# Optimization experiments

Measured on AMD Instinct MI355X. Metric: run time of the kernel, lower is better.

Reference implementation:

```python
import jax, jax.numpy as jnp
import numpy as np

N_NODES = 100000


def setup_inputs() -> dict:
    key = jax.random.key(0)
    k1, k2, k3, k4 = jax.random.split(key, 4)
    h = jax.random.normal(k1, (N_NODES, 128), dtype=jnp.float32)
    src = jax.random.randint(k2, (1600000,), 0, N_NODES, dtype=jnp.int32)
    dst = jax.random.randint(k3, (1600000,), 0, N_NODES, dtype=jnp.int32)
    # Linear params (PyTorch default init scale ~ 1/sqrt(in_feats))
    W = jax.random.normal(k4, (128, 128), dtype=jnp.float32) * (1.0 / np.sqrt(128.0))
    b = jnp.zeros((128,), dtype=jnp.float32)
    return {"h": h, "src": src, "dst": dst, "W": W, "b": b}


def reference(h, src, dst, W, b):
    # fn.copy_src: gather source-node features per edge  [E, F]
    msgs = h[src]
    # fn.sum: scatter-add messages into destination nodes  [N, F]
    agg = jax.ops.segment_sum(msgs, dst, num_segments=h.shape[0])
    # NodeUpdateModule: linear + relu
    out = agg @ W.T + b
    return jax.nn.relu(out)
```

## Files before the change

### kernel.cpp

```cpp
#include <hip/hip_runtime.h>

#define F     128
#define NPB   128
#define NPBS  7
#define CAP   6144
#define NBMAX 1024
#define SPLIT 4
#define NPG   32
#define ECAP  1024
#define BR    64
#define KC    32

typedef short bf16x8 __attribute__((ext_vector_type(8)));
typedef float f32x4  __attribute__((ext_vector_type(4)));

__device__ __forceinline__ unsigned short f32_to_bf16_rne(float x) {
    unsigned u = __float_as_uint(x);
    u += 0x7fffu + ((u >> 16) & 1u);
    return (unsigned short)(u >> 16);
}
__device__ __forceinline__ float bf16_to_f32(unsigned short u) {
    return __uint_as_float((unsigned)u << 16);
}

__global__ __launch_bounds__(256) void conv_w_kernel(
        const float* __restrict__ Wf, unsigned short* __restrict__ Wb, int n4) {
    int i = blockIdx.x * blockDim.x + threadIdx.x;
    if (i < n4) {
        float4 v = *(const float4*)(Wf + 4 * (long)i);
        ushort4 o;
        o.x = f32_to_bf16_rne(v.x);
        o.y = f32_to_bf16_rne(v.y);
        o.z = f32_to_bf16_rne(v.z);
        o.w = f32_to_bf16_rne(v.w);
        *(ushort4*)(Wb + 4 * (long)i) = o;
    }
}

__global__ __launch_bounds__(256) void gemm_h_kernel(
        const float* __restrict__ h,
        const unsigned short* __restrict__ Wb,
        unsigned short* __restrict__ hp,
        int n_rows) {
    const int wave = (blockIdx.x * 256 + threadIdx.x) >> 6;
    const int lane = threadIdx.x & 63;
    const int m0 = wave * 16;
    if (m0 >= n_rows) return;
    const int mn   = lane & 15;
    const int quad = lane >> 4;

    const int rowc = min(m0 + mn, n_rows - 1);
    const float* arow = h + (long)rowc * F + quad * 8;

    bf16x8 afr[4];
    #pragma unroll
    for (int kk = 0; kk < 4; ++kk) {
        float4 p0 = *(const float4*)(arow + kk * 32);
        float4 p1 = *(const float4*)(arow + kk * 32 + 4);
        bf16x8 f;
        f[0] = (short)f32_to_bf16_rne(p0.x);
        f[1] = (short)f32_to_bf16_rne(p0.y);
        f[2] = (short)f32_to_bf16_rne(p0.z);
        f[3] = (short)f32_to_bf16_rne(p0.w);
        f[4] = (short)f32_to_bf16_rne(p1.x);
        f[5] = (short)f32_to_bf16_rne(p1.y);
        f[6] = (short)f32_to_bf16_rne(p1.z);
        f[7] = (short)f32_to_bf16_rne(p1.w);
        afr[kk] = f;
    }

    f32x4 acc[8];
    #pragma unroll
    for (int t = 0; t < 8; ++t) acc[t] = (f32x4){0.f, 0.f, 0.f, 0.f};

    #pragma unroll
    for (int kk = 0; kk < 4; ++kk) {
        #pragma unroll
        for (int t = 0; t < 8; ++t) {
            const unsigned short* wp = Wb + (long)(t * 16 + mn) * F + kk * 32 + quad * 8;
            bf16x8 bfr = *(const bf16x8*)wp;
            acc[t] = __builtin_amdgcn_mfma_f32_16x16x32_bf16(afr[kk], bfr, acc[t], 0, 0, 0);
        }
    }

    #pragma unroll
    for (int t = 0; t < 8; ++t) {
        const int col = t * 16 + mn;
        #pragma unroll
        for (int r = 0; r < 4; ++r) {
            const int orow = m0 + quad * 4 + r;
            if (orow < n_rows)
                hp[(long)orow * F + col] = f32_to_bf16_rne(acc[t][r]);
        }
    }
}

__global__ __launch_bounds__(256) void build_buckets_kernel(
        const int* __restrict__ src,
        const int* __restrict__ dst,
        const unsigned short* __restrict__ hp,
        int* __restrict__ bcnt,
        int* __restrict__ bpool,
        float* __restrict__ out,
        int n_edges, int NB) {
    __shared__ int hist[NBMAX];
    __shared__ int basep[NBMAX];

    const int per = (n_edges + gridDim.x - 1) / gridDim.x;
    const int lo = blockIdx.x * per;
    const int hi = min(n_edges, lo + per);
    const int tid = threadIdx.x;

    for (int i = tid; i < NB; i += 256) hist[i] = 0;
    __syncthreads();

    for (int i = lo + tid; i < hi; i += 256)
        atomicAdd(&hist[dst[i] >> NPBS], 1);
    __syncthreads();

    for (int i = tid; i < NB; i += 256) {
        int c = hist[i];
        basep[i] = c ? atomicAdd(&bcnt[i], c) : 0;
        hist[i] = 0;
    }
    __syncthreads();

    for (int i = lo + tid; i < hi; i += 256) {
        int d = dst[i], s = src[i];
        int bk = d >> NPBS;
        int p = atomicAdd(&hist[bk], 1);
        long idx = (long)basep[bk] + p;
        if (idx < CAP) {
            bpool[(long)bk * CAP + idx] = ((d & (NPB - 1)) << 20) | s;
        } else {
            float* o = out + (long)d * F;
            const unsigned short* hr = hp + (long)s * F;
            for (int k = 0; k < F; ++k) unsafeAtomicAdd(o + k, bf16_to_f32(hr[k]));
        }
    }
}

__global__ __launch_bounds__(256) void bucket_gather_kernel(
        const unsigned short* __restrict__ hp,
        const int* __restrict__ bcnt,
        const int* __restrict__ bpool,
        const float* __restrict__ bias,
        float* __restrict__ out,
        int n_nodes) {
    __shared__ int ecnt[NPG];
    __shared__ int eofs[NPG];
    __shared__ int epos[NPG];
    __shared__ int elist[ECAP];
    __shared__ int sflag;

    const int bkt = blockIdx.x >> 2;
    const int qr  = blockIdx.x & 3;
    const int q0  = qr * NPG;
    const int nb0 = (bkt << NPBS) + q0;
    const int tid = threadIdx.x;

    const int total = bcnt[bkt];
    const int count = min(total, CAP);
    const int* bp = bpool + (long)bkt * CAP;

    if (tid < NPG) ecnt[tid] = 0;
    if (tid == 0) sflag = 0;
    __syncthreads();

    for (int i = tid; i < count; i += 256) {
        int nl = (bp[i] >> 20) - q0;
        if ((unsigned)nl < NPG) atomicAdd(&ecnt[nl], 1);
    }
    __syncthreads();

    if (tid < NPG) {
        int a = ecnt[tid];
        int s = a;
        #pragma unroll
        for (int d = 1; d < NPG; d <<= 1) {
            int t = __shfl_up(s, d);
            if (tid >= d) s += t;
        }
        eofs[tid] = s - a;
        epos[tid] = s - a;
    }
    __syncthreads();

    for (int i = tid; i < count; i += 256) {
        int e = bp[i];
        int nl = (e >> 20) - q0;
        if ((unsigned)nl < NPG) {
            int p = atomicAdd(&epos[nl], 1);
            int s = e & 0xFFFFF;
            if (p < ECAP) {
                elist[p] = s;
            } else {
                sflag = 1;
                float* o = out + ((long)((bkt << NPBS) + (e >> 20))) * F;
                const unsigned short* hr = hp + (long)s * F;
                for (int k = tid & 0; k < F; ++k)
                    unsafeAtomicAdd(o + k, bf16_to_f32(hr[k]));
            }
        }
    }
    __syncthreads();

    const int lane = tid & 63;
    const int w = tid >> 6;
    const bool ovf = (total > CAP) || (sflag != 0);
    const float2 bv = *(const float2*)(bias + (lane << 1));

    for (int nl = w; nl < NPG; nl += 4) {
        int n = nb0 + nl;
        if (n >= n_nodes) break;
        const int beg = eofs[nl];
        const int dend = min(beg + ecnt[nl], ECAP);

        float ax = 0.f, ay = 0.f;
        for (int i = beg; i < dend; i += 8) {
            unsigned v[8]; bool val[8];
            #pragma unroll
            for (int j = 0; j < 8; ++j) {
                val[j] = (i + j) < dend;
                int sid = elist[val[j] ? i + j : beg];
                v[j] = *(const unsigned*)(hp + ((long)sid << NPBS) + (lane << 1));
            }
            #pragma unroll
            for (int j = 0; j < 8; ++j) {
                if (val[j]) {
                    ax += __uint_as_float(v[j] << 16);
                    ay += __uint_as_float(v[j] & 0xffff0000u);
                }
            }
        }

        float* o = out + ((long)n << NPBS) + (lane << 1);
        if (ovf) {
            ax += unsafeAtomicAdd(o, 0.f);
            ay += unsafeAtomicAdd(o + 1, 0.f);
        }
        float rx = fmaxf(ax + bv.x, 0.f);
        float ry = fmaxf(ay + bv.y, 0.f);
        *(float2*)o = make_float2(rx, ry);
    }
}

__global__ void scatter_add_kernel(const float* __restrict__ h,
                                   const int* __restrict__ src,
                                   const int* __restrict__ dst,
                                   float* __restrict__ agg,
                                   long total) {
    long stride = (long)gridDim.x * blockDim.x;
    for (long i = (long)blockIdx.x * blockDim.x + threadIdx.x; i < total; i += stride) {
        int e    = (int)(i >> 5);
        int lane = (int)(i & 31);
        int s = src[e];
        int d = dst[e];
        float4 v = *(const float4*)(h + (long)s * F + (lane << 2));
        float* o = agg + (long)d * F + (lane << 2);
        unsafeAtomicAdd(o + 0, v.x);
        unsafeAtomicAdd(o + 1, v.y);
        unsafeAtomicAdd(o + 2, v.z);
        unsafeAtomicAdd(o + 3, v.w);
    }
}

__global__ __launch_bounds__(256) void gemm_bias_relu_inplace(
        float* __restrict__ out,
        const float* __restrict__ W,
        const float* __restrict__ bias,
        int n_rows) {
    __shared__ __align__(16) float a_t[KC][BR + 4];
    __shared__ __align__(16) float w_t[KC][F + 4];
    const int tid = threadIdx.x;
    const int tx = tid & 15;
    const int ty = tid >> 4;
    const int row0 = blockIdx.x * BR;
    float acc[4][8];
    #pragma unroll
    for (int i = 0; i < 4; ++i)
        #pragma unroll
        for (int j = 0; j < 8; ++j) acc[i][j] = 0.f;
    for (int kc = 0; kc < F; kc += KC) {
        #pragma unroll
        for (int p = 0; p < 2; ++p) {
            int q = tid + p * 256, r = q >> 3, kq = q & 7;
            int row = row0 + r;
            float4 v = make_float4(0.f, 0.f, 0.f, 0.f);
            if (row < n_rows) v = *(const float4*)(out + (long)row * F + kc + (kq << 2));
            a_t[kq * 4 + 0][r] = v.x; a_t[kq * 4 + 1][r] = v.y;
            a_t[kq * 4 + 2][r] = v.z; a_t[kq * 4 + 3][r] = v.w;
        }
        #pragma unroll
        for (int p = 0; p < 4; ++p) {
            int q = tid + p * 256, j = q >> 3, kq = q & 7;
            float4 v = *(const float4*)(W + (long)j * F + kc + (kq << 2));
            w_t[kq * 4 + 0][j] = v.x; w_t[kq * 4 + 1][j] = v.y;
            w_t[kq * 4 + 2][j] = v.z; w_t[kq * 4 + 3][j] = v.w;
        }
        __syncthreads();
        #pragma unroll
        for (int k = 0; k < KC; ++k) {
            float4 av = *(const float4*)&a_t[k][ty << 2];
            float4 w0 = *(const float4*)&w_t[k][tx << 2];
            float4 w1 = *(const float4*)&w_t[k][64 + (tx << 2)];
            float a4[4] = {av.x, av.y, av.z, av.w};
            float wv[8] = {w0.x, w0.y, w0.z, w0.w, w1.x, w1.y, w1.z, w1.w};
            #pragma unroll
            for (int i = 0; i < 4; ++i)
                #pragma unroll
                for (int j = 0; j < 8; ++j) acc[i][j] += a4[i] * wv[j];
        }
        __syncthreads();
    }
    float4 b0 = *(const float4*)(bias + (tx << 2));
    float4 b1 = *(const float4*)(bias + 64 + (tx << 2));
    #pragma unroll
    for (int i = 0; i < 4; ++i) {
        int row = row0 + (ty << 2) + i;
        if (row < n_rows) {
            float4 r0, r1;
            r0.x = fmaxf(acc[i][0] + b0.x, 0.f); r0.y = fmaxf(acc[i][1] + b0.y, 0.f);
            r0.z = fmaxf(acc[i][2] + b0.z, 0.f); r0.w = fmaxf(acc[i][3] + b0.w, 0.f);
            r1.x = fmaxf(acc[i][4] + b1.x, 0.f); r1.y = fmaxf(acc[i][5] + b1.y, 0.f);
            r1.z = fmaxf(acc[i][6] + b1.z, 0.f); r1.w = fmaxf(acc[i][7] + b1.w, 0.f);
            *(float4*)(out + (long)row * F + (tx << 2)) = r0;
            *(float4*)(out + (long)row * F + 64 + (tx << 2)) = r1;
        }
    }
}

extern "C" void kernel_launch(void* const* d_in, const int* in_sizes, int n_in,
                              void* d_out, int out_size, void* d_ws, size_t ws_size,
                              hipStream_t stream) {
    const float* h   = (const float*)d_in[0];
    const int*   src = (const int*)d_in[1];
    const int*   dst = (const int*)d_in[2];
    const float* W   = (const float*)d_in[3];
    const float* b   = (const float*)d_in[4];
    float* out = (float*)d_out;

    const int n_nodes = in_sizes[0] / F;
    const int n_edges = in_sizes[1];
    const int NB = (n_nodes + NPB - 1) >> NPBS;

    const size_t off_bcnt  = 0;
    const size_t off_bpool = 4096;
    const size_t off_hp    = off_bpool + (size_t)NB * CAP * sizeof(int);
    const size_t off_wb    = off_hp + (size_t)n_nodes * F * sizeof(unsigned short);
    const size_t need      = off_wb + (size_t)F * F * sizeof(unsigned short);

    if (ws_size >= need && n_nodes < (1 << 20) && NB <= NBMAX) {
        int* bcnt  = (int*)((char*)d_ws + off_bcnt);
        int* bpool = (int*)((char*)d_ws + off_bpool);
        unsigned short* hp = (unsigned short*)((char*)d_ws + off_hp);
        unsigned short* Wb = (unsigned short*)((char*)d_ws + off_wb);

        hipMemsetAsync(bcnt, 0, (size_t)NB * sizeof(int), stream);
        hipMemsetAsync(out, 0, (size_t)out_size * sizeof(float), stream);

        conv_w_kernel<<<(F * F / 4 + 255) / 256, 256, 0, stream>>>(W, Wb, F * F / 4);

        const int ggrid = (n_nodes + 63) / 64;
        gemm_h_kernel<<<ggrid, 256, 0, stream>>>(h, Wb, hp, n_nodes);

        build_buckets_kernel<<<512, 256, 0, stream>>>(
            src, dst, hp, bcnt, bpool, out, n_edges, NB);

        bucket_gather_kernel<<<NB * SPLIT, 256, 0, stream>>>(
            hp, bcnt, bpool, b, out, n_nodes);
    } else {
        hipMemsetAsync(out, 0, (size_t)out_size * sizeof(float), stream);
        scatter_add_kernel<<<16384, 256, 0, stream>>>(
            h, src, dst, out, (long)n_edges * 32);
        const int gblocks = (n_nodes + BR - 1) / BR;
        gemm_bias_relu_inplace<<<gblocks, 256, 0, stream>>>(out, W, b, n_nodes);
    }
}
```

Baseline: 263.8 us.

## Fuse bucket build with bf16 GEMM and defer overflow edges to gather

```diff
diff --git a/kernel.cpp b/kernel.cpp
--- a/kernel.cpp
+++ b/kernel.cpp
@@ -5,9 +5,11 @@
 #define NPBS  7
 #define CAP   6144
 #define NBMAX 1024
-#define SPLIT 4
-#define NPG   32
+#define NBUILD 512
+#define SPLIT 8
+#define NPG   16
 #define ECAP  1024
+#define OCAP  131072
 #define BR    64
 #define KC    32
 
@@ -19,123 +21,114 @@
     u += 0x7fffu + ((u >> 16) & 1u);
     return (unsigned short)(u >> 16);
 }
-__device__ __forceinline__ float bf16_to_f32(unsigned short u) {
-    return __uint_as_float((unsigned)u << 16);
-}
-
-__global__ __launch_bounds__(256) void conv_w_kernel(
-        const float* __restrict__ Wf, unsigned short* __restrict__ Wb, int n4) {
-    int i = blockIdx.x * blockDim.x + threadIdx.x;
-    if (i < n4) {
-        float4 v = *(const float4*)(Wf + 4 * (long)i);
-        ushort4 o;
-        o.x = f32_to_bf16_rne(v.x);
-        o.y = f32_to_bf16_rne(v.y);
-        o.z = f32_to_bf16_rne(v.z);
-        o.w = f32_to_bf16_rne(v.w);
-        *(ushort4*)(Wb + 4 * (long)i) = o;
-    }
-}
-
-__global__ __launch_bounds__(256) void gemm_h_kernel(
+
+__global__ __launch_bounds__(256) void fused_build_gemm(
         const float* __restrict__ h,
-        const unsigned short* __restrict__ Wb,
-        unsigned short* __restrict__ hp,
-        int n_rows) {
-    const int wave = (blockIdx.x * 256 + threadIdx.x) >> 6;
-    const int lane = threadIdx.x & 63;
-    const int m0 = wave * 16;
-    if (m0 >= n_rows) return;
-    const int mn   = lane & 15;
-    const int quad = lane >> 4;
-
-    const int rowc = min(m0 + mn, n_rows - 1);
-    const float* arow = h + (long)rowc * F + quad * 8;
-
-    bf16x8 afr[4];
-    #pragma unroll
-    for (int kk = 0; kk < 4; ++kk) {
-        float4 p0 = *(const float4*)(arow + kk * 32);
-        float4 p1 = *(const float4*)(arow + kk * 32 + 4);
-        bf16x8 f;
-        f[0] = (short)f32_to_bf16_rne(p0.x);
-        f[1] = (short)f32_to_bf16_rne(p0.y);
-        f[2] = (short)f32_to_bf16_rne(p0.z);
-        f[3] = (short)f32_to_bf16_rne(p0.w);
-        f[4] = (short)f32_to_bf16_rne(p1.x);
-        f[5] = (short)f32_to_bf16_rne(p1.y);
-        f[6] = (short)f32_to_bf16_rne(p1.z);
-        f[7] = (short)f32_to_bf16_rne(p1.w);
-        afr[kk] = f;
-    }
-
-    f32x4 acc[8];
-    #pragma unroll
-    for (int t = 0; t < 8; ++t) acc[t] = (f32x4){0.f, 0.f, 0.f, 0.f};
-
-    #pragma unroll
-    for (int kk = 0; kk < 4; ++kk) {
-        #pragma unroll
-        for (int t = 0; t < 8; ++t) {
-            const unsigned short* wp = Wb + (long)(t * 16 + mn) * F + kk * 32 + quad * 8;
-            bf16x8 bfr = *(const bf16x8*)wp;
-            acc[t] = __builtin_amdgcn_mfma_f32_16x16x32_bf16(afr[kk], bfr, acc[t], 0, 0, 0);
-        }
-    }
-
-    #pragma unroll
-    for (int t = 0; t < 8; ++t) {
-        const int col = t * 16 + mn;
-        #pragma unroll
-        for (int r = 0; r < 4; ++r) {
-            const int orow = m0 + quad * 4 + r;
-            if (orow < n_rows)
-                hp[(long)orow * F + col] = f32_to_bf16_rne(acc[t][r]);
-        }
-    }
-}
-
-__global__ __launch_bounds__(256) void build_buckets_kernel(
+        const float* __restrict__ W,
         const int* __restrict__ src,
         const int* __restrict__ dst,
-        const unsigned short* __restrict__ hp,
         int* __restrict__ bcnt,
         int* __restrict__ bpool,
-        float* __restrict__ out,
-        int n_edges, int NB) {
+        uint2* __restrict__ ovf_list,
+        unsigned short* __restrict__ hp,
+        int n_edges, int n_nodes, int NB) {
     __shared__ int hist[NBMAX];
     __shared__ int basep[NBMAX];
 
-    const int per = (n_edges + gridDim.x - 1) / gridDim.x;
-    const int lo = blockIdx.x * per;
-    const int hi = min(n_edges, lo + per);
-    const int tid = threadIdx.x;
-
-    for (int i = tid; i < NB; i += 256) hist[i] = 0;
-    __syncthreads();
-
-    for (int i = lo + tid; i < hi; i += 256)
-        atomicAdd(&hist[dst[i] >> NPBS], 1);
-    __syncthreads();
-
-    for (int i = tid; i < NB; i += 256) {
-        int c = hist[i];
-        basep[i] = c ? atomicAdd(&bcnt[i], c) : 0;
-        hist[i] = 0;
-    }
-    __syncthreads();
-
-    for (int i = lo + tid; i < hi; i += 256) {
-        int d = dst[i], s = src[i];
-        int bk = d >> NPBS;
-        int p = atomicAdd(&hist[bk], 1);
-        long idx = (long)basep[bk] + p;
-        if (idx < CAP) {
-            bpool[(long)bk * CAP + idx] = ((d & (NPB - 1)) << 20) | s;
-        } else {
-            float* o = out + (long)d * F;
-            const unsigned short* hr = hp + (long)s * F;
-            for (int k = 0; k < F; ++k) unsafeAtomicAdd(o + k, bf16_to_f32(hr[k]));
+    if (blockIdx.x < NBUILD) {
+        const int per = (n_edges + NBUILD - 1) / NBUILD;
+        const int lo = blockIdx.x * per;
+        const int hi = min(n_edges, lo + per);
+        const int tid = threadIdx.x;
+
+        for (int i = tid; i < NB; i += 256) hist[i] = 0;
+        __syncthreads();
+
+        for (int i = lo + tid; i < hi; i += 256)
+            atomicAdd(&hist[dst[i] >> NPBS], 1);
+        __syncthreads();
+
+        for (int i = tid; i < NB; i += 256) {
+            int c = hist[i];
+            basep[i] = c ? atomicAdd(&bcnt[i], c) : 0;
+            hist[i] = 0;
+        }
+        __syncthreads();
+
+        int* ovf_cnt = bcnt + NBMAX;
+        for (int i = lo + tid; i < hi; i += 256) {
+            int d = dst[i], s = src[i];
+            int bk = d >> NPBS;
+            int p = atomicAdd(&hist[bk], 1);
+            long idx = (long)basep[bk] + p;
+            if (idx < CAP) {
+                bpool[(long)bk * CAP + idx] = ((d & (NPB - 1)) << 20) | s;
+            } else {
+                int op = atomicAdd(ovf_cnt, 1);
+                if (op < OCAP) ovf_list[op] = make_uint2((unsigned)s, (unsigned)d);
+            }
+        }
+    } else {
+        const int wave = ((blockIdx.x - NBUILD) * 256 + (int)threadIdx.x) >> 6;
+        const int lane = threadIdx.x & 63;
+        const int m0 = wave * 16;
+        if (m0 >= n_nodes) return;
+        const int mn   = lane & 15;
+        const int quad = lane >> 4;
+
+        const int rowc = min(m0 + mn, n_nodes - 1);
+        const float* arow = h + (long)rowc * F + quad * 8;
+
+        bf16x8 afr[4];
+        #pragma unroll
+        for (int kk = 0; kk < 4; ++kk) {
+            float4 p0 = *(const float4*)(arow + kk * 32);
+            float4 p1 = *(const float4*)(arow + kk * 32 + 4);
+            bf16x8 f;
+            f[0] = (short)f32_to_bf16_rne(p0.x);
+            f[1] = (short)f32_to_bf16_rne(p0.y);
+            f[2] = (short)f32_to_bf16_rne(p0.z);
+            f[3] = (short)f32_to_bf16_rne(p0.w);
+            f[4] = (short)f32_to_bf16_rne(p1.x);
+            f[5] = (short)f32_to_bf16_rne(p1.y);
+            f[6] = (short)f32_to_bf16_rne(p1.z);
+            f[7] = (short)f32_to_bf16_rne(p1.w);
+            afr[kk] = f;
+        }
+
+        f32x4 acc[8];
+        #pragma unroll
+        for (int t = 0; t < 8; ++t) acc[t] = (f32x4){0.f, 0.f, 0.f, 0.f};
+
+        #pragma unroll
+        for (int kk = 0; kk < 4; ++kk) {
+            #pragma unroll
+            for (int t = 0; t < 8; ++t) {
+                const float* wp = W + (long)(t * 16 + mn) * F + kk * 32 + quad * 8;
+                float4 q0 = *(const float4*)wp;
+                float4 q1 = *(const float4*)(wp + 4);
+                bf16x8 bfr;
+                bfr[0] = (short)f32_to_bf16_rne(q0.x);
+                bfr[1] = (short)f32_to_bf16_rne(q0.y);
+                bfr[2] = (short)f32_to_bf16_rne(q0.z);
+                bfr[3] = (short)f32_to_bf16_rne(q0.w);
+                bfr[4] = (short)f32_to_bf16_rne(q1.x);
+                bfr[5] = (short)f32_to_bf16_rne(q1.y);
+                bfr[6] = (short)f32_to_bf16_rne(q1.z);
+                bfr[7] = (short)f32_to_bf16_rne(q1.w);
+                acc[t] = __builtin_amdgcn_mfma_f32_16x16x32_bf16(afr[kk], bfr, acc[t], 0, 0, 0);
+            }
+        }
+
+        #pragma unroll
+        for (int t = 0; t < 8; ++t) {
+            const int col = t * 16 + mn;
+            #pragma unroll
+            for (int r = 0; r < 4; ++r) {
+                const int orow = m0 + quad * 4 + r;
+                if (orow < n_nodes)
+                    hp[(long)orow * F + col] = f32_to_bf16_rne(acc[t][r]);
+            }
         }
     }
 }
@@ -143,6 +136,7 @@
 __global__ __launch_bounds__(256) void bucket_gather_kernel(
         const unsigned short* __restrict__ hp,
         const int* __restrict__ bcnt,
+        const uint2* __restrict__ ovf_list,
         const int* __restrict__ bpool,
         const float* __restrict__ bias,
         float* __restrict__ out,
@@ -151,11 +145,9 @@
     __shared__ int eofs[NPG];
     __shared__ int epos[NPG];
     __shared__ int elist[ECAP];
-    __shared__ int sflag;
-
-    const int bkt = blockIdx.x >> 2;
-    const int qr  = blockIdx.x & 3;
-    const int q0  = qr * NPG;
+
+    const int bkt = blockIdx.x >> 3;
+    const int q0  = (blockIdx.x & 7) * NPG;
     const int nb0 = (bkt << NPBS) + q0;
     const int tid = threadIdx.x;
 
@@ -164,7 +156,6 @@
     const int* bp = bpool + (long)bkt * CAP;
 
     if (tid < NPG) ecnt[tid] = 0;
-    if (tid == 0) sflag = 0;
     __syncthreads();
 
     for (int i = tid; i < count; i += 256) {
@@ -174,8 +165,7 @@
     __syncthreads();
 
     if (tid < NPG) {
-        int a = ecnt[tid];
-        int s = a;
+        int a = ecnt[tid], s = a;
         #pragma unroll
         for (int d = 1; d < NPG; d <<= 1) {
             int t = __shfl_up(s, d);
@@ -191,57 +181,69 @@
         int nl = (e >> 20) - q0;
         if ((unsigned)nl < NPG) {
             int p = atomicAdd(&epos[nl], 1);
-            int s = e & 0xFFFFF;
-            if (p < ECAP) {
-                elist[p] = s;
-            } else {
-                sflag = 1;
-                float* o = out + ((long)((bkt << NPBS) + (e >> 20))) * F;
-                const unsigned short* hr = hp + (long)s * F;
-                for (int k = tid & 0; k < F; ++k)
-                    unsafeAtomicAdd(o + k, bf16_to_f32(hr[k]));
-            }
+            if (p < ECAP) elist[p] = e & 0xFFFFF;
         }
     }
     __syncthreads();
 
     const int lane = tid & 63;
-    const int w = tid >> 6;
-    const bool ovf = (total > CAP) || (sflag != 0);
-    const float2 bv = *(const float2*)(bias + (lane << 1));
-
-    for (int nl = w; nl < NPG; nl += 4) {
-        int n = nb0 + nl;
-        if (n >= n_nodes) break;
-        const int beg = eofs[nl];
-        const int dend = min(beg + ecnt[nl], ECAP);
-
-        float ax = 0.f, ay = 0.f;
-        for (int i = beg; i < dend; i += 8) {
-            unsigned v[8]; bool val[8];
+    const int w    = tid >> 6;
+    const int half = lane >> 5;
+    const int sl   = lane & 31;
+    const int ovfn = min(bcnt[NBMAX], OCAP);
+    const float4 bv = *(const float4*)(bias + (sl << 2));
+
+    #pragma unroll
+    for (int pr = 0; pr < 2; ++pr) {
+        const int nl  = (w << 2) + (pr << 1) + half;
+        const int myn = nb0 + nl;
+        const bool act = myn < n_nodes;
+        const int mydeg = act ? ecnt[nl] : 0;
+        const int myoff = eofs[nl];
+        const int odeg = __shfl(mydeg, lane ^ 32);
+        const int dmax = max(mydeg, odeg);
+
+        float a0 = 0.f, a1 = 0.f, a2 = 0.f, a3 = 0.f;
+        for (int i = 0; i < dmax; i += 8) {
+            uint2 v[8]; bool val[8];
             #pragma unroll
             for (int j = 0; j < 8; ++j) {
-                val[j] = (i + j) < dend;
-                int sid = elist[val[j] ? i + j : beg];
-                v[j] = *(const unsigned*)(hp + ((long)sid << NPBS) + (lane << 1));
+                val[j] = (i + j) < mydeg;
+                int idx = min(myoff + (val[j] ? i + j : 0), ECAP - 1);
+                int sid = min(elist[idx], n_nodes - 1);
+                v[j] = *(const uint2*)(hp + ((long)sid << NPBS) + (sl << 2));
             }
             #pragma unroll
             for (int j = 0; j < 8; ++j) {
                 if (val[j]) {
-                    ax += __uint_as_float(v[j] << 16);
-                    ay += __uint_as_float(v[j] & 0xffff0000u);
+                    a0 += __uint_as_float(v[j].x << 16);
+                    a1 += __uint_as_float(v[j].x & 0xffff0000u);
+                    a2 += __uint_as_float(v[j].y << 16);
+                    a3 += __uint_as_float(v[j].y & 0xffff0000u);
                 }
             }
         }
 
-        float* o = out + ((long)n << NPBS) + (lane << 1);
-        if (ovf) {
-            ax += unsafeAtomicAdd(o, 0.f);
-            ay += unsafeAtomicAdd(o + 1, 0.f);
-        }
-        float rx = fmaxf(ax + bv.x, 0.f);
-        float ry = fmaxf(ay + bv.y, 0.f);
-        *(float2*)o = make_float2(rx, ry);
+        for (int i = 0; i < ovfn; ++i) {
+            uint2 e = ovf_list[i];
+            if (act && (int)e.y == myn) {
+                int sid = min((int)e.x, n_nodes - 1);
+                uint2 v = *(const uint2*)(hp + ((long)sid << NPBS) + (sl << 2));
+                a0 += __uint_as_float(v.x << 16);
+                a1 += __uint_as_float(v.x & 0xffff0000u);
+                a2 += __uint_as_float(v.y << 16);
+                a3 += __uint_as_float(v.y & 0xffff0000u);
+            }
+        }
+
+        if (act) {
+            float4 r;
+            r.x = fmaxf(a0 + bv.x, 0.f);
+            r.y = fmaxf(a1 + bv.y, 0.f);
+            r.z = fmaxf(a2 + bv.z, 0.f);
+            r.w = fmaxf(a3 + bv.w, 0.f);
+            *(float4*)(out + ((long)myn << NPBS) + (sl << 2)) = r;
+        }
     }
 }
 
@@ -344,31 +346,26 @@
     const int n_edges = in_sizes[1];
     const int NB = (n_nodes + NPB - 1) >> NPBS;
 
-    const size_t off_bcnt  = 0;
-    const size_t off_bpool = 4096;
-    const size_t off_hp    = off_bpool + (size_t)NB * CAP * sizeof(int);
-    const size_t off_wb    = off_hp + (size_t)n_nodes * F * sizeof(unsigned short);
-    const size_t need      = off_wb + (size_t)F * F * sizeof(unsigned short);
+    const size_t off_bcnt = 0;
+    const size_t off_bpool = 8192;
+    const size_t off_ovf  = off_bpool + (size_t)NB * CAP * sizeof(int);
+    const size_t off_hp   = off_ovf + (size_t)OCAP * sizeof(uint2);
+    const size_t need     = off_hp + (size_t)n_nodes * F * sizeof(unsigned short);
 
     if (ws_size >= need && n_nodes < (1 << 20) && NB <= NBMAX) {
-        int* bcnt  = (int*)((char*)d_ws + off_bcnt);
-        int* bpool = (int*)((char*)d_ws + off_bpool);
+        int* bcnt   = (int*)((char*)d_ws + off_bcnt);
+        int* bpool  = (int*)((char*)d_ws + off_bpool);
+        uint2* ovfl = (uint2*)((char*)d_ws + off_ovf);
         unsigned short* hp = (unsigned short*)((char*)d_ws + off_hp);
-        unsigned short* Wb = (unsigned short*)((char*)d_ws + off_wb);
-
-        hipMemsetAsync(bcnt, 0, (size_t)NB * sizeof(int), stream);
-        hipMemsetAsync(out, 0, (size_t)out_size * sizeof(float), stream);
-
-        conv_w_kernel<<<(F * F / 4 + 255) / 256, 256, 0, stream>>>(W, Wb, F * F / 4);
-
-        const int ggrid = (n_nodes + 63) / 64;
-        gemm_h_kernel<<<ggrid, 256, 0, stream>>>(h, Wb, hp, n_nodes);
-
-        build_buckets_kernel<<<512, 256, 0, stream>>>(
-            src, dst, hp, bcnt, bpool, out, n_edges, NB);
+
+        hipMemsetAsync(bcnt, 0, (size_t)(NBMAX + 1) * sizeof(int), stream);
+
+        const int ngemm = (n_nodes + 63) / 64;
+        fused_build_gemm<<<NBUILD + ngemm, 256, 0, stream>>>(
+            h, W, src, dst, bcnt, bpool, ovfl, hp, n_edges, n_nodes, NB);
 
         bucket_gather_kernel<<<NB * SPLIT, 256, 0, stream>>>(
-            hp, bcnt, bpool, b, out, n_nodes);
+            hp, bcnt, ovfl, bpool, b, out, n_nodes);
     } else {
         hipMemsetAsync(out, 0, (size_t)out_size * sizeof(float), stream);
         scatter_add_kernel<<<16384, 256, 0, stream>>>(
```

After: 267.0 us. About the same (+1.2%).
